# Kernel tuning notes

Measured on AMD Instinct MI355X. Metric: run time of the kernel, lower is better.

Reference implementation:

```python
import jax, jax.numpy as jnp
import numpy as np

B, H, W = 4, 180, 180
C_L, C_C, C_OUT = 128, 128, 256
CH_ALL = 2 * (C_L + C_C)        # 512
CH_HID = CH_ALL // 3            # 170


def setup_inputs() -> dict:
    key = jax.random.key(0)
    ks = jax.random.split(key, 12)
    N = 160000
    inp = {
        'lidar_features': jax.random.normal(ks[0], (N, C_L), dtype=jnp.float32),
        'img_bev': jax.random.normal(ks[1], (B, C_C, H, W), dtype=jnp.float32),
        'batch_idx': jnp.sort(jax.random.randint(ks[2], (N,), 0, B, dtype=jnp.int32)),
        'y_idx': jax.random.randint(ks[3], (N,), 0, H, dtype=jnp.int32),
        'x_idx': jax.random.randint(ks[4], (N,), 0, W, dtype=jnp.int32),
        # weights stored as [in, out] (x @ W), equivalent to torch Linear weight.T
        'Wl1': jax.random.normal(ks[5], (CH_ALL, CH_HID), dtype=jnp.float32) * 0.02,
        'Wl2': jax.random.normal(ks[6], (CH_HID, C_L), dtype=jnp.float32) * 0.02,
        'Wc1': jax.random.normal(ks[7], (CH_ALL, CH_HID), dtype=jnp.float32) * 0.02,
        'Wc2': jax.random.normal(ks[8], (CH_HID, C_C), dtype=jnp.float32) * 0.02,
        'Wf1': jax.random.normal(ks[9], (C_L + C_C, C_OUT), dtype=jnp.float32) * 0.02,
        'Wf2': jax.random.normal(ks[10], (C_OUT, C_OUT), dtype=jnp.float32) * 0.02,
    }
    return inp


def reference(lidar_features, img_bev, Wl1, Wl2, Wc1, Wc2, Wf1, Wf2,
              batch_idx, y_idx, x_idx):
    relu = jax.nn.relu
    spatial_size = H * W
    # flatten dense image BEV map: [B,C,H,W] -> [B*H*W, C]
    img_flat = jnp.transpose(img_bev, (0, 2, 3, 1)).reshape(B * H * W, C_C)
    # per-voxel flat row index (faithful to original incl. clamp to spatial_size-2)
    row = batch_idx * spatial_size + y_idx * W + x_idx
    row = jnp.clip(row, 0, spatial_size - 2)
    cam_feat = img_flat[row]                                  # [N, C_C] gather
    # per-batch segment min/max (ragged reduction)
    lmin = jax.ops.segment_min(lidar_features, batch_idx, num_segments=B)
    lmax = jax.ops.segment_max(lidar_features, batch_idx, num_segments=B)
    cmin = jax.ops.segment_min(cam_feat, batch_idx, num_segments=B)
    cmax = jax.ops.segment_max(cam_feat, batch_idx, num_segments=B)
    cat_mm = jnp.concatenate([lmin, lmax, cmin, cmax], axis=-1)   # [B, 512]
    att_l = jax.nn.sigmoid(relu(relu(cat_mm @ Wl1) @ Wl2))        # [B, C_L]
    att_c = jax.nn.sigmoid(relu(relu(cat_mm @ Wc1) @ Wc2))        # [B, C_C]
    gated_l = lidar_features * att_l[batch_idx]
    gated_c = cam_feat * att_c[batch_idx]
    fused = jnp.concatenate([gated_l, gated_c], axis=-1)          # [N, 256]
    out = relu(relu(fused @ Wf1) @ Wf2)                           # [N, 256]
    return out
```

## Files before the change

### kernel.cpp

```cpp
#include <hip/hip_runtime.h>
#include <math.h>

#define NB 4
#define HH 180
#define WWW 180
#define SPATIAL (HH*WWW)
#define CH_HID 170
#define CLAMP_ROW (SPATIAL-2)

typedef short v8s __attribute__((ext_vector_type(8)));
typedef short v4s __attribute__((ext_vector_type(4)));
typedef float v4f __attribute__((ext_vector_type(4)));

__device__ __forceinline__ unsigned fmap(float f) {
    unsigned u = __float_as_uint(f);
    return (u & 0x80000000u) ? ~u : (u | 0x80000000u);
}
__device__ __forceinline__ float funmap(unsigned u) {
    unsigned b = (u & 0x80000000u) ? (u & 0x7FFFFFFFu) : ~u;
    return __uint_as_float(b);
}
__device__ __forceinline__ unsigned short f2bf(float f) {
    unsigned u = __float_as_uint(f);
    u += 0x7FFFu + ((u >> 16) & 1);
    return (unsigned short)(u >> 16);
}

__global__ void k_prep(const float* __restrict__ Wf1, const float* __restrict__ Wf2,
                       unsigned short* __restrict__ W1S, unsigned short* __restrict__ W2S,
                       unsigned* __restrict__ stats) {
    if (blockIdx.y == 0 && blockIdx.x < 8) {
        int i = blockIdx.x * 256 + threadIdx.x;
        int j = i & 511;
        bool is_min = (j < 128) || (j >= 256 && j < 384);
        stats[i] = is_min ? 0xFFFFFFFFu : 0u;
    }
    const float* W = blockIdx.y ? Wf2 : Wf1;
    unsigned short* WS = blockIdx.y ? W2S : W1S;
    const int tid = threadIdx.x;
    const int frag = blockIdx.x * 4 + (tid >> 6);
    const int lane = tid & 63;
    const int nt = frag >> 3, ks = frag & 7;
    const int q = lane >> 4, ml = lane & 15;
    v8s pk;
    #pragma unroll
    for (int j = 0; j < 8; ++j)
        pk[j] = (short)f2bf(W[(ks*32 + q*8 + j)*256 + nt*16 + ml]);
    *(v8s*)&WS[(frag*64 + lane)*8] = pk;
}

__global__ void k_setup(const float* __restrict__ img, float* __restrict__ camT) {
    __shared__ float tile[32][33];
    int s0 = blockIdx.x * 32, c0 = blockIdx.y * 32;
    int lx = threadIdx.x & 31, ly = threadIdx.x >> 5;
    for (int i = 0; i < 4; ++i) {
        int s = s0 + lx;
        if (s < SPATIAL)
            tile[ly + i*8][lx] = img[(c0 + ly + i*8) * SPATIAL + s];
    }
    __syncthreads();
    for (int i = 0; i < 4; ++i) {
        int s = s0 + ly + i*8;
        if (s < SPATIAL)
            camT[s*128 + c0 + lx] = tile[lx][ly + i*8];
    }
}

__global__ __launch_bounds__(256)
void k_reduce(const float* __restrict__ lidar, const float* __restrict__ camT,
              const int* __restrict__ bidx, const int* __restrict__ yidx,
              const int* __restrict__ xidx,
              unsigned* __restrict__ stats, int N, int chunk) {
    __shared__ int sb[256];
    __shared__ int srow[256];
    __shared__ v4f redmn[4][64];
    __shared__ v4f redmx[4][64];
    const int tid = threadIdx.x;
    const int vbeg = blockIdx.x * chunk;
    const int cnt = min(chunk, N - vbeg);
    if (cnt <= 0) return;
    if (tid < cnt) {
        int v = vbeg + tid;
        sb[tid] = bidx[v];
        srow[tid] = min(yidx[v]*WWW + xidx[v] + sb[tid]*SPATIAL, CLAMP_ROW);
    }
    __syncthreads();

    const int sub = tid >> 6;
    const int lane = tid & 63;
    const int c4 = lane * 4;
    const bool cam = (c4 >= 128);
    const int cc = cam ? (c4 - 128) : c4;
    const int min_off = cam ? (c4 + 128) : c4;

    const int b_first = sb[0], b_last = sb[cnt - 1];
    int s0 = 0;
    for (int bb = b_first; bb <= b_last; ++bb) {
        int s1 = cnt;
        if (bb < b_last) {
            int lo = s0, hi = cnt;
            while (lo < hi) { int mid = (lo + hi) >> 1; if (sb[mid] > bb) hi = mid; else lo = mid + 1; }
            s1 = lo;
        }
        float mn0 = INFINITY, mn1 = INFINITY, mn2 = INFINITY, mn3 = INFINITY;
        float mx0 = -INFINITY, mx1 = -INFINITY, mx2 = -INFINITY, mx3 = -INFINITY;
        const bool skipload = cam && (bb > 0);
        if (!skipload) {
            #pragma unroll 4
            for (int idx = s0 + sub; idx < s1; idx += 4) {
                const float* src = cam ? &camT[(size_t)srow[idx]*128 + cc]
                                       : &lidar[(size_t)(vbeg + idx)*128 + c4];
                v4f val = *(const v4f*)src;
                mn0 = fminf(mn0, val[0]); mx0 = fmaxf(mx0, val[0]);
                mn1 = fminf(mn1, val[1]); mx1 = fmaxf(mx1, val[1]);
                mn2 = fminf(mn2, val[2]); mx2 = fmaxf(mx2, val[2]);
                mn3 = fminf(mn3, val[3]); mx3 = fmaxf(mx3, val[3]);
            }
        } else {
            v4f cv = *(const v4f*)&camT[(size_t)CLAMP_ROW*128 + cc];
            mn0 = mx0 = cv[0]; mn1 = mx1 = cv[1]; mn2 = mx2 = cv[2]; mn3 = mx3 = cv[3];
        }
        redmn[sub][lane] = (v4f){mn0, mn1, mn2, mn3};
        redmx[sub][lane] = (v4f){mx0, mx1, mx2, mx3};
        __syncthreads();
        if (sub == 0) {
            v4f a0 = redmn[0][lane], a1 = redmn[1][lane], a2 = redmn[2][lane], a3 = redmn[3][lane];
            v4f b0 = redmx[0][lane], b1 = redmx[1][lane], b2 = redmx[2][lane], b3 = redmx[3][lane];
            int base = bb*512 + min_off;
            for (int j = 0; j < 4; ++j) {
                float mn = fminf(fminf(a0[j], a1[j]), fminf(a2[j], a3[j]));
                float mx = fmaxf(fmaxf(b0[j], b1[j]), fmaxf(b2[j], b3[j]));
                atomicMin(&stats[base + j], fmap(mn));
                atomicMax(&stats[base + 128 + j], fmap(mx));
            }
        }
        __syncthreads();
        s0 = s1;
    }
}

__global__ void k_mlp(const unsigned* __restrict__ stats,
                      const float* __restrict__ Wl1, const float* __restrict__ Wl2,
                      const float* __restrict__ Wc1, const float* __restrict__ Wc2,
                      float* __restrict__ att) {
    __shared__ float cat[512];
    __shared__ float hid[CH_HID];
    int b = blockIdx.x >> 1;
    int net = blockIdx.x & 1;
    const float* W1 = net ? Wc1 : Wl1;
    const float* W2 = net ? Wc2 : Wl2;
    int tid = threadIdx.x;
    for (int j = tid; j < 512; j += 256) cat[j] = funmap(stats[b*512 + j]);
    __syncthreads();
    if (tid < CH_HID) {
        float s = 0.f;
        #pragma unroll 16
        for (int k = 0; k < 512; ++k) s += cat[k] * W1[k*CH_HID + tid];
        hid[tid] = fmaxf(s, 0.f);
    }
    __syncthreads();
    if (tid < 128) {
        float s = 0.f;
        #pragma unroll 10
        for (int k = 0; k < CH_HID; ++k) s += hid[k] * W2[k*128 + tid];
        s = fmaxf(s, 0.f);
        att[b*256 + net*128 + tid] = 1.f / (1.f + expf(-s));
    }
}

__global__ __launch_bounds__(256, 3)
void k_main(const float* __restrict__ lidar, const float* __restrict__ camT,
            const int* __restrict__ bidx, const int* __restrict__ yidx,
            const int* __restrict__ xidx, const float* __restrict__ att,
            const unsigned short* __restrict__ W1S, const unsigned short* __restrict__ W2S,
            float* __restrict__ out, int N) {
    __shared__ __align__(16) char smem[64 * 264 * 2];
    unsigned short (*sA)[264] = (unsigned short(*)[264])smem;
    float* sAf = (float*)smem;
    __shared__ int srow[64];
    __shared__ int sbb[64];
    const int tid = threadIdx.x;
    const int v0 = blockIdx.x * 64;

    if (tid < 64) {
        int v = v0 + tid;
        int b = 0, row = 0;
        if (v < N) {
            b = bidx[v];
            row = min(b*SPATIAL + yidx[v]*WWW + xidx[v], CLAMP_ROW);
        }
        sbb[tid] = b;
        srow[tid] = row;
    }
    const int c = (tid & 63) * 4;
    const bool cam = (c >= 128);
    v4f attv0 = *(const v4f*)&att[0*256 + c];
    v4f attv1 = *(const v4f*)&att[1*256 + c];
    v4f attv2 = *(const v4f*)&att[2*256 + c];
    v4f attv3 = *(const v4f*)&att[3*256 + c];
    __syncthreads();

    #pragma unroll
    for (int half = 0; half < 2; ++half) {
        v4f x[8]; int bm[8];
        #pragma unroll
        for (int j = 0; j < 8; ++j) {
            int m = (half*8 + j)*4 + (tid >> 6);
            int vc = min(v0 + m, N - 1);
            bm[j] = sbb[m];
            const float* src = cam ? &camT[(size_t)srow[m]*128 + (c - 128)]
                                   : &lidar[(size_t)vc*128 + c];
            x[j] = *(const v4f*)src;
        }
        #pragma unroll
        for (int j = 0; j < 8; ++j) {
            int m = (half*8 + j)*4 + (tid >> 6);
            int b = bm[j];
            v4f a = attv0;
            if (b == 1) a = attv1;
            if (b == 2) a = attv2;
            if (b == 3) a = attv3;
            v4f val = x[j] * a;
            v4s pk;
            #pragma unroll
            for (int jj = 0; jj < 4; ++jj) pk[jj] = (short)f2bf(val[jj]);
            *(v4s*)&sA[m][c] = pk;
        }
    }

    const int wave = tid >> 6;
    const int lane = tid & 63;
    const int ml = lane & 15;
    const int q = lane >> 4;

    v4f acc[4][4];
    for (int layer = 0; layer < 2; ++layer) {
        const unsigned short* WS = layer ? W2S : W1S;
        const v4f zz = {0.f, 0.f, 0.f, 0.f};
        for (int rt = 0; rt < 4; ++rt)
            for (int ct = 0; ct < 4; ++ct) acc[rt][ct] = zz;

        __syncthreads();
        #pragma unroll
        for (int ks = 0; ks < 8; ++ks) {
            v8s a[4];
            const int ka = ks*32 + q*8;
            #pragma unroll
            for (int rt = 0; rt < 4; ++rt)
                a[rt] = *(const v8s*)&sA[rt*16 + ml][ka];
            #pragma unroll
            for (int ct = 0; ct < 4; ++ct) {
                v8s bfr = *(const v8s*)&WS[(((wave*4 + ct)*8 + ks)*64 + lane)*8];
                #pragma unroll
                for (int rt = 0; rt < 4; ++rt)
                    acc[rt][ct] = __builtin_amdgcn_mfma_f32_16x16x32_bf16(
                        a[rt], bfr, acc[rt][ct], 0, 0, 0);
            }
        }
        __syncthreads();
        if (layer == 0) {
            for (int rt = 0; rt < 4; ++rt)
                for (int ct = 0; ct < 4; ++ct)
                    for (int r = 0; r < 4; ++r)
                        sA[rt*16 + q*4 + r][wave*64 + ct*16 + ml] =
                            f2bf(fmaxf(acc[rt][ct][r], 0.f));
        }
    }

    const int c4 = (tid & 63) * 4;
    #pragma unroll
    for (int p = 0; p < 2; ++p) {
        __syncthreads();
        #pragma unroll
        for (int rt = 2*p; rt < 2*p + 2; ++rt)
            for (int ct = 0; ct < 4; ++ct)
                for (int r = 0; r < 4; ++r)
                    sAf[((rt - 2*p)*16 + q*4 + r)*260 + wave*64 + ct*16 + ml] =
                        fmaxf(acc[rt][ct][r], 0.f);
        __syncthreads();
        #pragma unroll
        for (int i = 0; i < 8; ++i) {
            int rl = (tid >> 6) + i*4;
            int v = v0 + p*32 + rl;
            if (v < N)
                *(v4f*)&out[(size_t)v*256 + c4] = *(const v4f*)&sAf[rl*260 + c4];
        }
    }
}

extern "C" void kernel_launch(void* const* d_in, const int* in_sizes, int n_in,
                              void* d_out, int out_size, void* d_ws, size_t ws_size,
                              hipStream_t stream) {
    const float* lidar = (const float*)d_in[0];
    const float* img   = (const float*)d_in[1];
    const int*   bidx  = (const int*)d_in[2];
    const int*   yidx  = (const int*)d_in[3];
    const int*   xidx  = (const int*)d_in[4];
    const float* Wl1   = (const float*)d_in[5];
    const float* Wl2   = (const float*)d_in[6];
    const float* Wc1   = (const float*)d_in[7];
    const float* Wc2   = (const float*)d_in[8];
    const float* Wf1   = (const float*)d_in[9];
    const float* Wf2   = (const float*)d_in[10];
    float* out = (float*)d_out;
    const int N = in_sizes[0] / 128;

    unsigned* stats = (unsigned*)d_ws;
    float* att = (float*)((char*)d_ws + 8192);
    unsigned short* W1S = (unsigned short*)((char*)d_ws + 16384);
    unsigned short* W2S = (unsigned short*)((char*)d_ws + 16384 + 131072);
    float* camT = (float*)((char*)d_ws + 16384 + 262144);

    k_prep<<<dim3(32, 2), 256, 0, stream>>>(Wf1, Wf2, W1S, W2S, stats);
    k_setup<<<dim3((SPATIAL + 31) / 32, 4), 256, 0, stream>>>(img, camT);
    const int rblocks = 2560;
    const int chunk = (N + rblocks - 1) / rblocks;
    k_reduce<<<rblocks, 256, 0, stream>>>(lidar, camT, bidx, yidx, xidx, stats, N, chunk);
    k_mlp<<<8, 256, 0, stream>>>(stats, Wl1, Wl2, Wc1, Wc2, att);
    k_main<<<(N + 63) / 64, 256, 0, stream>>>(lidar, camT, bidx, yidx, xidx, att, W1S, W2S, out, N);
}
```

Baseline: 443.3 us.

## Split segment reduction into grid-stride lidar pass and batch-0 camera pass

The reduction kernel is split into two block roles. The first role streams lidar features with a grid-stride loop and keeps per-batch min/max accumulators in registers with predicated updates. The second role gathers camera rows only for batch-0 voxels, because for later batches the clamped row is constant. The MLP kernel now reads that constant camera row directly for batches 1-3 instead of the stats buffer, and k_main's launch bounds rise to 4 waves per SIMD. Predicated per-batch accumulation uses more registers and ALU work per element, and the higher occupancy target may cause spills in k_main.

Result: slower. 453.4 us (+2.3%).

```diff
diff --git a/kernel.cpp b/kernel.cpp
--- a/kernel.cpp
+++ b/kernel.cpp
@@ -24,6 +24,12 @@
     unsigned u = __float_as_uint(f);
     u += 0x7FFFu + ((u >> 16) & 1);
     return (unsigned short)(u >> 16);
+}
+__device__ __forceinline__ v4f vmin4(v4f a, v4f b) {
+    v4f r; r[0]=fminf(a[0],b[0]); r[1]=fminf(a[1],b[1]); r[2]=fminf(a[2],b[2]); r[3]=fminf(a[3],b[3]); return r;
+}
+__device__ __forceinline__ v4f vmax4(v4f a, v4f b) {
+    v4f r; r[0]=fmaxf(a[0],b[0]); r[1]=fmaxf(a[1],b[1]); r[2]=fmaxf(a[2],b[2]); r[3]=fmaxf(a[3],b[3]); return r;
 }
 
 __global__ void k_prep(const float* __restrict__ Wf1, const float* __restrict__ Wf2,
@@ -70,76 +76,110 @@
 void k_reduce(const float* __restrict__ lidar, const float* __restrict__ camT,
               const int* __restrict__ bidx, const int* __restrict__ yidx,
               const int* __restrict__ xidx,
-              unsigned* __restrict__ stats, int N, int chunk) {
-    __shared__ int sb[256];
-    __shared__ int srow[256];
-    __shared__ v4f redmn[4][64];
-    __shared__ v4f redmx[4][64];
+              unsigned* __restrict__ stats, int N, int nblkA, int chunkB) {
+    __shared__ __align__(16) char sm[32768];
     const int tid = threadIdx.x;
-    const int vbeg = blockIdx.x * chunk;
-    const int cnt = min(chunk, N - vbeg);
-    if (cnt <= 0) return;
-    if (tid < cnt) {
-        int v = vbeg + tid;
-        sb[tid] = bidx[v];
-        srow[tid] = min(yidx[v]*WWW + xidx[v] + sb[tid]*SPATIAL, CLAMP_ROW);
-    }
-    __syncthreads();
-
-    const int sub = tid >> 6;
-    const int lane = tid & 63;
-    const int c4 = lane * 4;
-    const bool cam = (c4 >= 128);
-    const int cc = cam ? (c4 - 128) : c4;
-    const int min_off = cam ? (c4 + 128) : c4;
-
-    const int b_first = sb[0], b_last = sb[cnt - 1];
-    int s0 = 0;
-    for (int bb = b_first; bb <= b_last; ++bb) {
-        int s1 = cnt;
-        if (bb < b_last) {
-            int lo = s0, hi = cnt;
-            while (lo < hi) { int mid = (lo + hi) >> 1; if (sb[mid] > bb) hi = mid; else lo = mid + 1; }
-            s1 = lo;
-        }
-        float mn0 = INFINITY, mn1 = INFINITY, mn2 = INFINITY, mn3 = INFINITY;
-        float mx0 = -INFINITY, mx1 = -INFINITY, mx2 = -INFINITY, mx3 = -INFINITY;
-        const bool skipload = cam && (bb > 0);
-        if (!skipload) {
-            #pragma unroll 4
-            for (int idx = s0 + sub; idx < s1; idx += 4) {
-                const float* src = cam ? &camT[(size_t)srow[idx]*128 + cc]
-                                       : &lidar[(size_t)(vbeg + idx)*128 + c4];
-                v4f val = *(const v4f*)src;
-                mn0 = fminf(mn0, val[0]); mx0 = fmaxf(mx0, val[0]);
-                mn1 = fminf(mn1, val[1]); mx1 = fmaxf(mx1, val[1]);
-                mn2 = fminf(mn2, val[2]); mx2 = fmaxf(mx2, val[2]);
-                mn3 = fminf(mn3, val[3]); mx3 = fmaxf(mx3, val[3]);
+
+    if ((int)blockIdx.x < nblkA) {
+        v4f (*red)[8][32] = (v4f(*)[8][32])sm;
+        const int total = N * 32;
+        const int stride = nblkA * 256;
+        const v4f pinf = {INFINITY, INFINITY, INFINITY, INFINITY};
+        const v4f ninf = {-INFINITY, -INFINITY, -INFINITY, -INFINITY};
+        v4f mn0 = pinf, mn1 = pinf, mn2 = pinf, mn3 = pinf;
+        v4f mx0 = ninf, mx1 = ninf, mx2 = ninf, mx3 = ninf;
+
+        #define ACCUM(vv, bb) do { \
+            bool m0_ = ((bb) == 0), m1_ = ((bb) == 1), m2_ = ((bb) == 2), m3_ = ((bb) == 3); \
+            mn0 = m0_ ? vmin4(mn0, (vv)) : mn0;  mx0 = m0_ ? vmax4(mx0, (vv)) : mx0; \
+            mn1 = m1_ ? vmin4(mn1, (vv)) : mn1;  mx1 = m1_ ? vmax4(mx1, (vv)) : mx1; \
+            mn2 = m2_ ? vmin4(mn2, (vv)) : mn2;  mx2 = m2_ ? vmax4(mx2, (vv)) : mx2; \
+            mn3 = m3_ ? vmin4(mn3, (vv)) : mn3;  mx3 = m3_ ? vmax4(mx3, (vv)) : mx3; \
+        } while (0)
+
+        int i = blockIdx.x * 256 + tid;
+        for (; i + 3 * stride < total; i += 4 * stride) {
+            v4f x0 = *(const v4f*)&lidar[(size_t)i * 4];
+            v4f x1 = *(const v4f*)&lidar[(size_t)(i + stride) * 4];
+            v4f x2 = *(const v4f*)&lidar[(size_t)(i + 2 * stride) * 4];
+            v4f x3 = *(const v4f*)&lidar[(size_t)(i + 3 * stride) * 4];
+            int b0 = bidx[i >> 5];
+            int b1 = bidx[(i + stride) >> 5];
+            int b2 = bidx[(i + 2 * stride) >> 5];
+            int b3 = bidx[(i + 3 * stride) >> 5];
+            ACCUM(x0, b0); ACCUM(x1, b1); ACCUM(x2, b2); ACCUM(x3, b3);
+        }
+        for (; i < total; i += stride) {
+            v4f x = *(const v4f*)&lidar[(size_t)i * 4];
+            int b = bidx[i >> 5];
+            ACCUM(x, b);
+        }
+        #undef ACCUM
+
+        const int sub = tid >> 5, cc = tid & 31;
+        red[sub][0][cc] = mn0; red[sub][1][cc] = mx0;
+        red[sub][2][cc] = mn1; red[sub][3][cc] = mx1;
+        red[sub][4][cc] = mn2; red[sub][5][cc] = mx2;
+        red[sub][6][cc] = mn3; red[sub][7][cc] = mx3;
+        __syncthreads();
+        const int acc = tid >> 5;
+        const bool ismax = acc & 1;
+        v4f r = red[0][acc][cc];
+        #pragma unroll
+        for (int s = 1; s < 8; ++s)
+            r = ismax ? vmax4(r, red[s][acc][cc]) : vmin4(r, red[s][acc][cc]);
+        const int b = acc >> 1;
+        const int off = b * 512 + (ismax ? 128 : 0) + cc * 4;
+        #pragma unroll
+        for (int j = 0; j < 4; ++j) {
+            if (ismax) atomicMax(&stats[off + j], fmap(r[j]));
+            else       atomicMin(&stats[off + j], fmap(r[j]));
+        }
+    } else {
+        int* srow = (int*)sm;
+        v4f (*cred)[2][32] = (v4f(*)[2][32])(sm + 2048);
+        const int blk = blockIdx.x - nblkA;
+        const int vbeg = blk * chunkB;
+        const int cnt = min(chunkB, N - vbeg);
+        if (cnt <= 0) return;
+        if (bidx[vbeg] != 0) return;
+        if (tid < cnt) {
+            int v = vbeg + tid;
+            srow[tid] = (bidx[v] == 0) ? min(yidx[v] * WWW + xidx[v], CLAMP_ROW) : -1;
+        }
+        __syncthreads();
+        const int c4 = (tid & 31) * 4;
+        v4f mn = {INFINITY, INFINITY, INFINITY, INFINITY};
+        v4f mx = {-INFINITY, -INFINITY, -INFINITY, -INFINITY};
+        for (int idx = tid >> 5; idx < cnt; idx += 8) {
+            int r = srow[idx];
+            if (r >= 0) {
+                v4f v = *(const v4f*)&camT[(size_t)r * 128 + c4];
+                mn = vmin4(mn, v);
+                mx = vmax4(mx, v);
             }
-        } else {
-            v4f cv = *(const v4f*)&camT[(size_t)CLAMP_ROW*128 + cc];
-            mn0 = mx0 = cv[0]; mn1 = mx1 = cv[1]; mn2 = mx2 = cv[2]; mn3 = mx3 = cv[3];
-        }
-        redmn[sub][lane] = (v4f){mn0, mn1, mn2, mn3};
-        redmx[sub][lane] = (v4f){mx0, mx1, mx2, mx3};
-        __syncthreads();
-        if (sub == 0) {
-            v4f a0 = redmn[0][lane], a1 = redmn[1][lane], a2 = redmn[2][lane], a3 = redmn[3][lane];
-            v4f b0 = redmx[0][lane], b1 = redmx[1][lane], b2 = redmx[2][lane], b3 = redmx[3][lane];
-            int base = bb*512 + min_off;
+        }
+        const int sub = tid >> 5, cc = tid & 31;
+        cred[sub][0][cc] = mn;
+        cred[sub][1][cc] = mx;
+        __syncthreads();
+        if (tid < 64) {
+            const bool ismax = tid >= 32;
+            v4f r = cred[0][ismax][cc];
+            #pragma unroll
+            for (int s = 1; s < 8; ++s)
+                r = ismax ? vmax4(r, cred[s][ismax][cc]) : vmin4(r, cred[s][ismax][cc]);
+            const int off = 256 + (ismax ? 128 : 0) + cc * 4;
+            #pragma unroll
             for (int j = 0; j < 4; ++j) {
-                float mn = fminf(fminf(a0[j], a1[j]), fminf(a2[j], a3[j]));
-                float mx = fmaxf(fmaxf(b0[j], b1[j]), fmaxf(b2[j], b3[j]));
-                atomicMin(&stats[base + j], fmap(mn));
-                atomicMax(&stats[base + 128 + j], fmap(mx));
+                if (ismax) atomicMax(&stats[off + j], fmap(r[j]));
+                else       atomicMin(&stats[off + j], fmap(r[j]));
             }
         }
-        __syncthreads();
-        s0 = s1;
-    }
-}
-
-__global__ void k_mlp(const unsigned* __restrict__ stats,
+    }
+}
+
+__global__ void k_mlp(const unsigned* __restrict__ stats, const float* __restrict__ camT,
                       const float* __restrict__ Wl1, const float* __restrict__ Wl2,
                       const float* __restrict__ Wc1, const float* __restrict__ Wc2,
                       float* __restrict__ att) {
@@ -150,7 +190,12 @@
     const float* W1 = net ? Wc1 : Wl1;
     const float* W2 = net ? Wc2 : Wl2;
     int tid = threadIdx.x;
-    for (int j = tid; j < 512; j += 256) cat[j] = funmap(stats[b*512 + j]);
+    for (int j = tid; j < 512; j += 256) {
+        float x;
+        if (j < 256 || b == 0) x = funmap(stats[b * 512 + j]);
+        else                   x = camT[(size_t)CLAMP_ROW * 128 + (j & 127)];
+        cat[j] = x;
+    }
     __syncthreads();
     if (tid < CH_HID) {
         float s = 0.f;
@@ -168,7 +213,7 @@
     }
 }
 
-__global__ __launch_bounds__(256, 3)
+__global__ __launch_bounds__(256, 4)
 void k_main(const float* __restrict__ lidar, const float* __restrict__ camT,
             const int* __restrict__ bidx, const int* __restrict__ yidx,
             const int* __restrict__ xidx, const float* __restrict__ att,
@@ -313,9 +358,10 @@
 
     k_prep<<<dim3(32, 2), 256, 0, stream>>>(Wf1, Wf2, W1S, W2S, stats);
     k_setup<<<dim3((SPATIAL + 31) / 32, 4), 256, 0, stream>>>(img, camT);
-    const int rblocks = 2560;
-    const int chunk = (N + rblocks - 1) / rblocks;
-    k_reduce<<<rblocks, 256, 0, stream>>>(lidar, camT, bidx, yidx, xidx, stats, N, chunk);
-    k_mlp<<<8, 256, 0, stream>>>(stats, Wl1, Wl2, Wc1, Wc2, att);
+    const int nblkA = 1024;
+    const int chunkB = 256;
+    const int nblkB = (N + chunkB - 1) / chunkB;
+    k_reduce<<<nblkA + nblkB, 256, 0, stream>>>(lidar, camT, bidx, yidx, xidx, stats, N, nblkA, chunkB);
+    k_mlp<<<8, 256, 0, stream>>>(stats, camT, Wl1, Wl2, Wc1, Wc2, att);
     k_main<<<(N + 63) / 64, 256, 0, stream>>>(lidar, camT, bidx, yidx, xidx, att, W1S, W2S, out, N);
 }
```
